# Kernel tuning notes

Measured on AMD Instinct MI355X. Metric: run time of the kernel, lower is better.

## Reference

```python
import jax, jax.numpy as jnp
import numpy as np

N, E, IN, HID, H, C, NL, OUT = 50000, 500000, 384, 128, 8, 16, 3, 16
NEG_SLOPE = 0.2

def setup_inputs() -> dict:
    key = jax.random.key(0)
    ks = jax.random.split(key, 16)
    s = 0.1
    return {
        "x": jax.random.normal(ks[0], (N, IN), jnp.float32),
        "edge_index": jax.random.randint(ks[1], (2, E), 0, N, jnp.int32),
        "proj_w": jax.random.normal(ks[2], (IN, HID), jnp.float32) * s,
        "proj_b": jax.random.normal(ks[3], (HID,), jnp.float32) * s,
        "lin_w": jax.random.normal(ks[4], (NL, HID, HID), jnp.float32) * s,
        "att_src": jax.random.normal(ks[5], (NL, H, C), jnp.float32) * s,
        "att_dst": jax.random.normal(ks[6], (NL, H, C), jnp.float32) * s,
        "gat_b": jax.random.normal(ks[7], (NL, HID), jnp.float32) * s,
        "ln_g": jnp.ones((NL, HID), jnp.float32),
        "ln_b": jnp.zeros((NL, HID), jnp.float32),
        "cls_w1": jax.random.normal(ks[8], (HID, HID // 2), jnp.float32) * s,
        "cls_b1": jax.random.normal(ks[9], (HID // 2,), jnp.float32) * s,
        "cls_w2": jax.random.normal(ks[10], (HID // 2, OUT), jnp.float32) * s,
        "cls_b2": jax.random.normal(ks[11], (OUT,), jnp.float32) * s,
    }

def _layernorm(h, g, b, eps=1e-5):
    mu = jnp.mean(h, axis=-1, keepdims=True)
    var = jnp.var(h, axis=-1, keepdims=True)
    return (h - mu) * jax.lax.rsqrt(var + eps) * g + b

def _gat_layer(h, src, dst, w, a_src, a_dst, bias):
    # h: [N, HID]; per-head transform -> [N, H, C]
    xh = (h @ w).reshape(N, H, C)
    al_s = jnp.einsum('nhc,hc->nh', xh, a_src)   # [N, H]
    al_d = jnp.einsum('nhc,hc->nh', xh, a_dst)
    e = jax.nn.leaky_relu(al_s[src] + al_d[dst], NEG_SLOPE)  # [E+N, H]
    # segment softmax over incoming edges of each dst node
    m = jax.ops.segment_max(e, dst, num_segments=N)
    e = jnp.exp(e - m[dst])
    denom = jax.ops.segment_sum(e, dst, num_segments=N)
    alpha = e / (denom[dst] + 1e-16)
    msg = xh[src] * alpha[:, :, None]            # [E+N, H, C]
    out = jax.ops.segment_sum(msg, dst, num_segments=N)
    return out.reshape(N, H * C) + bias

def reference(x, edge_index, proj_w, proj_b, lin_w, att_src, att_dst, gat_b,
              ln_g, ln_b, cls_w1, cls_b1, cls_w2, cls_b2):
    loops = jnp.arange(N, dtype=edge_index.dtype)  # PyG GATConv adds self-loops
    src = jnp.concatenate([edge_index[0], loops])
    dst = jnp.concatenate([edge_index[1], loops])
    h = jax.nn.relu(x @ proj_w + proj_b)
    for l in range(NL):
        h_res = h
        h = _gat_layer(h, src, dst, lin_w[l], att_src[l], att_dst[l], gat_b[l])
        h = h + h_res
        h = jax.nn.relu(_layernorm(h, ln_g[l], ln_b[l]))
    logits = jax.nn.relu(h @ cls_w1 + cls_b1) @ cls_w2 + cls_b2
    return jax.nn.log_softmax(logits, axis=1)
```

## Files before the change

### kernel.cpp

```cpp
#include <hip/hip_runtime.h>
#include <hip/hip_bf16.h>
#include <math.h>

#define NN 50000
#define EE 500000
#define DIN 384
#define HIDD 128
#define NHEAD 8
#define OUTD 16

typedef __attribute__((ext_vector_type(8))) __bf16 bf16x8;
typedef __attribute__((ext_vector_type(4))) float f32x4;

__device__ __forceinline__ ushort f2bf(float f) {
  union { float f; unsigned u; } v; v.f = f;
  unsigned r = v.u + 0x7fffu + ((v.u >> 16) & 1u);
  return (ushort)(r >> 16);
}
__device__ __forceinline__ float bflo(unsigned w) {
  union { unsigned u; float f; } v; v.u = w << 16; return v.f;
}
__device__ __forceinline__ float bfhi(unsigned w) {
  union { unsigned u; float f; } v; v.u = w & 0xffff0000u; return v.f;
}

__global__ void zero_ints(int* p, int n) {
  int i = blockIdx.x * blockDim.x + threadIdx.x;
  if (i < n) p[i] = 0;
}

__global__ void hist_kernel(const int* __restrict__ dst, int* __restrict__ counts, int e) {
  int i = blockIdx.x * blockDim.x + threadIdx.x;
  if (i < e) atomicAdd(&counts[dst[i]], 1);
}

#define SCAN_BS 256
#define SCAN_NBLK ((NN + SCAN_BS - 1) / SCAN_BS)

__global__ __launch_bounds__(256) void partial_sums(const int* __restrict__ counts,
                                                    int* __restrict__ bsum, int n) {
  __shared__ int red[256];
  int i = blockIdx.x * 256 + threadIdx.x;
  red[threadIdx.x] = (i < n) ? counts[i] : 0;
  __syncthreads();
  #pragma unroll
  for (int off = 128; off; off >>= 1) {
    if (threadIdx.x < off) red[threadIdx.x] += red[threadIdx.x + off];
    __syncthreads();
  }
  if (threadIdx.x == 0) bsum[blockIdx.x] = red[0];
}

__global__ __launch_bounds__(256) void scan_bsums(const int* __restrict__ bsum,
                                                  int* __restrict__ boff, int nb) {
  __shared__ int buf[256];
  int t = threadIdx.x;
  int v = (t < nb) ? bsum[t] : 0;
  buf[t] = v;
  __syncthreads();
  #pragma unroll
  for (int off = 1; off < 256; off <<= 1) {
    int u = (t >= off) ? buf[t - off] : 0;
    __syncthreads();
    buf[t] += u;
    __syncthreads();
  }
  if (t < nb) boff[t] = buf[t] - v;
}

__global__ __launch_bounds__(256) void final_scan(const int* __restrict__ counts,
                                                  const int* __restrict__ boff,
                                                  int* __restrict__ rowptr,
                                                  int* __restrict__ woff, int n) {
  __shared__ int buf[256];
  int i = blockIdx.x * 256 + threadIdx.x;
  int t = threadIdx.x;
  int v = (i < n) ? counts[i] : 0;
  buf[t] = v;
  __syncthreads();
  #pragma unroll
  for (int off = 1; off < 256; off <<= 1) {
    int u = (t >= off) ? buf[t - off] : 0;
    __syncthreads();
    buf[t] += u;
    __syncthreads();
  }
  int excl = boff[blockIdx.x] + buf[t] - v;
  if (i < n) { rowptr[i] = excl; woff[i] = excl; }
  if (i == n - 1) rowptr[n] = excl + v;
}

__global__ void scatter_kernel(const int* __restrict__ src, const int* __restrict__ dst,
                               int* __restrict__ woff, int* __restrict__ col, int e) {
  int i = blockIdx.x * blockDim.x + threadIdx.x;
  if (i < e) {
    int p = atomicAdd(&woff[dst[i]], 1);
    col[p] = src[i];
  }
}

__global__ void prep_weights(const float* __restrict__ proj_w,
                             const float* __restrict__ lin_w,
                             const float* __restrict__ cls_w1,
                             const float* __restrict__ cls_w2,
                             ushort* __restrict__ wt) {
  int i = blockIdx.x * blockDim.x + threadIdx.x;
  if (i < 49152) {
    int k = i >> 7, n = i & 127;
    wt[n * 384 + k] = f2bf(proj_w[i]);
  } else if (i < 98304) {
    int j = i - 49152;
    int l = j >> 14, rem = j & 16383;
    int k = rem >> 7, n = rem & 127;
    wt[49152 + l * 16384 + n * 128 + k] = f2bf(lin_w[j]);
  } else if (i < 106496) {
    int j = i - 98304;
    int n = j >> 7, k = j & 127;
    wt[98304 + n * 128 + k] = f2bf(cls_w1[k * 64 + n]);
  } else if (i < 107520) {
    int j = i - 106496;
    int n = j >> 6, k = j & 63;
    wt[106496 + n * 64 + k] = f2bf(cls_w2[k * 16 + n]);
  }
}

#define LDS_STRIDE 72
template<bool RELU_BIAS, bool OUTBF>
__global__ __launch_bounds__(256) void mfma_gemm_n128(const float* __restrict__ A,
                                                      const ushort* __restrict__ Bt,
                                                      const float* __restrict__ bias,
                                                      void* __restrict__ Cv, int M, int K) {
  __shared__ ushort sA[128 * LDS_STRIDE];
  __shared__ ushort sB[128 * LDS_STRIDE];
  const int tid = threadIdx.x;
  const int wave = tid >> 6, lane = tid & 63;
  const int q = lane >> 4, lm = lane & 15;
  const int wr = wave >> 1, wc = wave & 1;
  const int m0 = blockIdx.x * 128;

  f32x4 acc[4][4];
  #pragma unroll
  for (int i = 0; i < 4; i++)
    #pragma unroll
    for (int j = 0; j < 4; j++) acc[i][j] = {0.f, 0.f, 0.f, 0.f};

  for (int k0 = 0; k0 < K; k0 += 64) {
    __syncthreads();
    #pragma unroll
    for (int p = 0; p < 8; ++p) {
      int idx = p * 256 + tid;
      int r = idx >> 4;
      int c = (idx & 15) << 2;
      float4 v = make_float4(0.f, 0.f, 0.f, 0.f);
      if (m0 + r < M) v = *(const float4*)(A + (size_t)(m0 + r) * K + k0 + c);
      ushort4 u;
      u.x = f2bf(v.x); u.y = f2bf(v.y); u.z = f2bf(v.z); u.w = f2bf(v.w);
      *(ushort4*)&sA[r * LDS_STRIDE + c] = u;
    }
    #pragma unroll
    for (int p = 0; p < 4; ++p) {
      int idx = p * 256 + tid;
      int r = idx >> 3;
      int c = (idx & 7) << 3;
      bf16x8 v = *(const bf16x8*)(Bt + (size_t)r * K + k0 + c);
      *(bf16x8*)&sB[r * LDS_STRIDE + c] = v;
    }
    __syncthreads();
    #pragma unroll
    for (int ks = 0; ks < 2; ++ks) {
      bf16x8 af[4], bfv[4];
      #pragma unroll
      for (int t = 0; t < 4; ++t) {
        af[t]  = *(const bf16x8*)&sA[(wr * 64 + t * 16 + lm) * LDS_STRIDE + ks * 32 + q * 8];
        bfv[t] = *(const bf16x8*)&sB[(wc * 64 + t * 16 + lm) * LDS_STRIDE + ks * 32 + q * 8];
      }
      #pragma unroll
      for (int i = 0; i < 4; ++i)
        #pragma unroll
        for (int j = 0; j < 4; ++j)
          acc[i][j] = __builtin_amdgcn_mfma_f32_16x16x32_bf16(af[i], bfv[j], acc[i][j], 0, 0, 0);
    }
  }
  #pragma unroll
  for (int i = 0; i < 4; ++i) {
    #pragma unroll
    for (int r = 0; r < 4; ++r) {
      int row = m0 + wr * 64 + i * 16 + q * 4 + r;
      if (row < M) {
        #pragma unroll
        for (int j = 0; j < 4; ++j) {
          int colc = wc * 64 + j * 16 + lm;
          float v = acc[i][j][r];
          if (RELU_BIAS) { v += bias[colc]; v = fmaxf(v, 0.f); }
          if (OUTBF) ((ushort*)Cv)[(size_t)row * 128 + colc] = f2bf(v);
          else       ((float*)Cv)[(size_t)row * 128 + colc] = v;
        }
      }
    }
  }
}

__global__ void att_logits_kernel(const ushort* __restrict__ xh,
                                  const float* __restrict__ att_s,
                                  const float* __restrict__ att_d,
                                  float* __restrict__ al_s, float* __restrict__ al_d, int n) {
  int t = blockIdx.x * blockDim.x + threadIdx.x;
  if (t >= n * NHEAD) return;
  int head = t & 7;
  const unsigned* xw = (const unsigned*)(xh + (size_t)t * 16);
  const float* as = att_s + head * 16;
  const float* ad = att_d + head * 16;
  float ss = 0.f, dd = 0.f;
  #pragma unroll
  for (int i = 0; i < 8; ++i) {
    unsigned w = xw[i];
    float x0 = bflo(w), x1 = bfhi(w);
    ss = fmaf(x0, as[i * 2], fmaf(x1, as[i * 2 + 1], ss));
    dd = fmaf(x0, ad[i * 2], fmaf(x1, ad[i * 2 + 1], dd));
  }
  al_s[t] = ss;
  al_d[t] = dd;
}

__global__ __launch_bounds__(256) void gat_aggregate(
    const ushort* __restrict__ xh, const float* __restrict__ al_s,
    const float* __restrict__ al_d, const int* __restrict__ rowptr,
    const int* __restrict__ col, const float* __restrict__ h_res,
    const float* __restrict__ gb, const float* __restrict__ lng,
    const float* __restrict__ lnb, float* __restrict__ h_out, int n) {
  const int lane = threadIdx.x & 63;
  const int node = (blockIdx.x * blockDim.x + threadIdx.x) >> 6;
  if (node >= n) return;
  const int e8 = lane >> 3;
  const int hh = lane & 7;
  const int head = lane >> 3;
  const unsigned* xw_base = (const unsigned*)xh;

  const int start = rowptr[node], end = rowptr[node + 1];
  const int T = end - start + 1;
  const float ald_c = al_d[node * 8 + hh];

  float m = -INFINITY, denom = 0.f, acc0 = 0.f, acc1 = 0.f;

  for (int c = 0; c < T; c += 8) {
    int it = c + e8;
    bool valid = it < T;
    int idx = start + it;
    int s = (valid && idx < end) ? col[idx] : node;
    float e = al_s[s * 8 + hh] + ald_c;
    e = (e > 0.f) ? e : 0.2f * e;
    if (!valid) e = -INFINITY;
    float cm = e;
    cm = fmaxf(cm, __shfl_xor(cm, 8));
    cm = fmaxf(cm, __shfl_xor(cm, 16));
    cm = fmaxf(cm, __shfl_xor(cm, 32));
    float newm = fmaxf(m, __shfl(cm, head));
    float newm_c = __shfl(newm, hh * 8);
    float p_lane = __expf(e - newm_c);
    float scale = __expf(m - newm);
    m = newm;
    unsigned xg[8];
    int sj[8];
    #pragma unroll
    for (int j = 0; j < 8; ++j) sj[j] = __shfl(s, j * 8);
    #pragma unroll
    for (int j = 0; j < 8; ++j) xg[j] = xw_base[(size_t)sj[j] * 64 + lane];
    denom *= scale; acc0 *= scale; acc1 *= scale;
    #pragma unroll
    for (int j = 0; j < 8; ++j) {
      float pj = __shfl(p_lane, j * 8 + head);
      denom += pj;
      acc0 = fmaf(pj, bflo(xg[j]), acc0);
      acc1 = fmaf(pj, bfhi(xg[j]), acc1);
    }
  }

  float inv = 1.f / denom;
  int c0 = lane * 2, c1 = c0 + 1;
  float2 hr = ((const float2*)h_res)[(size_t)node * 64 + lane];
  float v0 = acc0 * inv + gb[c0] + hr.x;
  float v1 = acc1 * inv + gb[c1] + hr.y;
  float sum = v0 + v1;
  #pragma unroll
  for (int off = 32; off; off >>= 1) sum += __shfl_xor(sum, off);
  float mean = sum * (1.f / 128.f);
  float d0 = v0 - mean, d1 = v1 - mean;
  float sq = d0 * d0 + d1 * d1;
  #pragma unroll
  for (int off = 32; off; off >>= 1) sq += __shfl_xor(sq, off);
  float rstd = rsqrtf(sq * (1.f / 128.f) + 1e-5f);
  float o0 = fmaxf(d0 * rstd * lng[c0] + lnb[c0], 0.f);
  float o1 = fmaxf(d1 * rstd * lng[c1] + lnb[c1], 0.f);
  ((float2*)h_out)[(size_t)node * 64 + lane] = make_float2(o0, o1);
}

#define CSTR 136
#define HSTR 72
__global__ __launch_bounds__(256) void classifier_mfma(
    const float* __restrict__ h, const ushort* __restrict__ w1t,
    const float* __restrict__ b1, const ushort* __restrict__ w2t,
    const float* __restrict__ b2, float* __restrict__ out, int n) {
  __shared__ ushort sA[128 * CSTR];
  __shared__ ushort sB[64 * CSTR];
  __shared__ ushort sHid[128 * HSTR];
  const int tid = threadIdx.x;
  const int wave = tid >> 6, lane = tid & 63;
  const int q = lane >> 4, lm = lane & 15;
  const int wr = wave >> 1, wc = wave & 1;
  const int m0 = blockIdx.x * 128;

  #pragma unroll
  for (int p = 0; p < 16; ++p) {
    int idx = p * 256 + tid;
    int r = idx >> 5;
    int c = (idx & 31) << 2;
    float4 v = make_float4(0.f, 0.f, 0.f, 0.f);
    if (m0 + r < n) v = *(const float4*)(h + (size_t)(m0 + r) * 128 + c);
    ushort4 u;
    u.x = f2bf(v.x); u.y = f2bf(v.y); u.z = f2bf(v.z); u.w = f2bf(v.w);
    *(ushort4*)&sA[r * CSTR + c] = u;
  }
  #pragma unroll
  for (int p = 0; p < 4; ++p) {
    int idx = p * 256 + tid;
    int r = idx >> 4;
    int c = (idx & 15) << 3;
    *(bf16x8*)&sB[r * CSTR + c] = *(const bf16x8*)(w1t + r * 128 + c);
  }
  __syncthreads();

  f32x4 acc[4][2];
  #pragma unroll
  for (int i = 0; i < 4; ++i)
    #pragma unroll
    for (int j = 0; j < 2; ++j) acc[i][j] = {0.f, 0.f, 0.f, 0.f};
  #pragma unroll
  for (int ks = 0; ks < 4; ++ks) {
    bf16x8 af[4], bfv[2];
    #pragma unroll
    for (int t = 0; t < 4; ++t)
      af[t] = *(const bf16x8*)&sA[(wr * 64 + t * 16 + lm) * CSTR + ks * 32 + q * 8];
    #pragma unroll
    for (int j = 0; j < 2; ++j)
      bfv[j] = *(const bf16x8*)&sB[(wc * 32 + j * 16 + lm) * CSTR + ks * 32 + q * 8];
    #pragma unroll
    for (int i = 0; i < 4; ++i)
      #pragma unroll
      for (int j = 0; j < 2; ++j)
        acc[i][j] = __builtin_amdgcn_mfma_f32_16x16x32_bf16(af[i], bfv[j], acc[i][j], 0, 0, 0);
  }
  #pragma unroll
  for (int i = 0; i < 4; ++i) {
    #pragma unroll
    for (int j = 0; j < 2; ++j) {
      int colc = wc * 32 + j * 16 + lm;
      float bb = b1[colc];
      #pragma unroll
      for (int r = 0; r < 4; ++r) {
        int row = wr * 64 + i * 16 + q * 4 + r;
        float v = fmaxf(acc[i][j][r] + bb, 0.f);
        sHid[row * HSTR + colc] = f2bf(v);
      }
    }
  }
  __syncthreads();

  f32x4 acc2[2] = {{0.f, 0.f, 0.f, 0.f}, {0.f, 0.f, 0.f, 0.f}};
  #pragma unroll
  for (int ks = 0; ks < 2; ++ks) {
    bf16x8 b2f = *(const bf16x8*)(w2t + lm * 64 + ks * 32 + q * 8);
    #pragma unroll
    for (int t = 0; t < 2; ++t) {
      bf16x8 a2 = *(const bf16x8*)&sHid[(wave * 32 + t * 16 + lm) * HSTR + ks * 32 + q * 8];
      acc2[t] = __builtin_amdgcn_mfma_f32_16x16x32_bf16(a2, b2f, acc2[t], 0, 0, 0);
    }
  }
  float bb2 = b2[lm];
  #pragma unroll
  for (int t = 0; t < 2; ++t) {
    #pragma unroll
    for (int r = 0; r < 4; ++r) {
      int row = m0 + wave * 32 + t * 16 + q * 4 + r;
      float lg = acc2[t][r] + bb2;
      float mx = lg;
      #pragma unroll
      for (int off = 8; off; off >>= 1) mx = fmaxf(mx, __shfl_xor(mx, off, 16));
      float se = __expf(lg - mx);
      #pragma unroll
      for (int off = 8; off; off >>= 1) se += __shfl_xor(se, off, 16);
      if (row < n) out[(size_t)row * 16 + lm] = lg - mx - __logf(se);
    }
  }
}

extern "C" void kernel_launch(void* const* d_in, const int* in_sizes, int n_in,
                              void* d_out, int out_size, void* d_ws, size_t ws_size,
                              hipStream_t stream) {
  const float* x       = (const float*)d_in[0];
  const int*   ei      = (const int*)d_in[1];
  const float* proj_w  = (const float*)d_in[2];
  const float* proj_b  = (const float*)d_in[3];
  const float* lin_w   = (const float*)d_in[4];
  const float* att_src = (const float*)d_in[5];
  const float* att_dst = (const float*)d_in[6];
  const float* gat_b   = (const float*)d_in[7];
  const float* ln_g    = (const float*)d_in[8];
  const float* ln_b    = (const float*)d_in[9];
  const float* cls_w1  = (const float*)d_in[10];
  const float* cls_b1  = (const float*)d_in[11];
  const float* cls_w2  = (const float*)d_in[12];
  const float* cls_b2  = (const float*)d_in[13];
  float* outp = (float*)d_out;

  const int N = NN, E = EE;
  ushort* wt   = (ushort*)d_ws;
  float* h0    = (float*)d_ws + 54272;
  float* h1    = h0 + (size_t)N * 128;
  ushort* xh_u = (ushort*)(h1 + (size_t)N * 128);
  float* als   = (float*)(xh_u + (size_t)N * 128);
  float* ald   = als + (size_t)N * NHEAD;
  int* counts  = (int*)(ald + (size_t)N * NHEAD);
  int* rowptr  = counts + N;
  int* woff    = rowptr + N + 1;
  int* col     = woff + N;
  int* bsum    = col + E;
  int* boff    = bsum + SCAN_NBLK;

  const int* e_src = ei;
  const int* e_dst = ei + E;

  prep_weights<<<(107520 + 255) / 256, 256, 0, stream>>>(proj_w, lin_w, cls_w1, cls_w2, wt);

  zero_ints<<<(N + 255) / 256, 256, 0, stream>>>(counts, N);
  hist_kernel<<<(E + 255) / 256, 256, 0, stream>>>(e_dst, counts, E);
  partial_sums<<<SCAN_NBLK, 256, 0, stream>>>(counts, bsum, N);
  scan_bsums<<<1, 256, 0, stream>>>(bsum, boff, SCAN_NBLK);
  final_scan<<<SCAN_NBLK, 256, 0, stream>>>(counts, boff, rowptr, woff, N);
  scatter_kernel<<<(E + 255) / 256, 256, 0, stream>>>(e_src, e_dst, woff, col, E);

  const int gblocks = (N + 127) / 128;
  mfma_gemm_n128<true, false><<<gblocks, 256, 0, stream>>>(x, wt, proj_b, h0, N, DIN);

  float* hc = h0;
  float* hn = h1;
  for (int l = 0; l < 3; ++l) {
    mfma_gemm_n128<false, true><<<gblocks, 256, 0, stream>>>(
        hc, wt + 49152 + l * 16384, nullptr, xh_u, N, 128);
    att_logits_kernel<<<(N * NHEAD + 255) / 256, 256, 0, stream>>>(
        xh_u, att_src + l * 128, att_dst + l * 128, als, ald, N);
    gat_aggregate<<<(N + 3) / 4, 256, 0, stream>>>(
        xh_u, als, ald, rowptr, col, hc, gat_b + l * 128, ln_g + l * 128,
        ln_b + l * 128, hn, N);
    float* t = hc; hc = hn; hn = t;
  }
  classifier_mfma<<<gblocks, 256, 0, stream>>>(hc, wt + 98304, cls_b1, wt + 106496, cls_b2, outp, N);
}
```

Baseline: 405.8 us.

## Store hidden activations in bf16 and shrink GEMM row tile to 64

Hidden-state buffers h0/h1 are now stored as bf16 instead of fp32, so the GEMMs, the aggregate residual read and output write, and the classifier all move half the bytes. The GEMM kernel is templated on input type and uses a 64-row tile, which doubles the block count for better occupancy across CUs. Out-of-range rows are clamped instead of branched. This adds bf16 rounding on the residual path, which may cost some accuracy.

```diff
diff --git a/kernel.cpp b/kernel.cpp
--- a/kernel.cpp
+++ b/kernel.cpp
@@ -125,75 +125,86 @@
 }
 
 #define LDS_STRIDE 72
-template<bool RELU_BIAS, bool OUTBF>
-__global__ __launch_bounds__(256) void mfma_gemm_n128(const float* __restrict__ A,
-                                                      const ushort* __restrict__ Bt,
-                                                      const float* __restrict__ bias,
-                                                      void* __restrict__ Cv, int M, int K) {
-  __shared__ ushort sA[128 * LDS_STRIDE];
+template<typename AT, bool RELU_BIAS>
+__global__ __launch_bounds__(256) void mfma_gemm64(const AT* __restrict__ A,
+                                                   const ushort* __restrict__ Bt,
+                                                   const float* __restrict__ bias,
+                                                   ushort* __restrict__ C, int M, int K) {
+  __shared__ ushort sA[64 * LDS_STRIDE];
   __shared__ ushort sB[128 * LDS_STRIDE];
   const int tid = threadIdx.x;
   const int wave = tid >> 6, lane = tid & 63;
   const int q = lane >> 4, lm = lane & 15;
   const int wr = wave >> 1, wc = wave & 1;
-  const int m0 = blockIdx.x * 128;
-
-  f32x4 acc[4][4];
-  #pragma unroll
-  for (int i = 0; i < 4; i++)
+  const int m0 = blockIdx.x * 64;
+
+  f32x4 acc[2][4];
+  #pragma unroll
+  for (int i = 0; i < 2; i++)
     #pragma unroll
     for (int j = 0; j < 4; j++) acc[i][j] = {0.f, 0.f, 0.f, 0.f};
 
   for (int k0 = 0; k0 < K; k0 += 64) {
     __syncthreads();
-    #pragma unroll
-    for (int p = 0; p < 8; ++p) {
-      int idx = p * 256 + tid;
-      int r = idx >> 4;
-      int c = (idx & 15) << 2;
-      float4 v = make_float4(0.f, 0.f, 0.f, 0.f);
-      if (m0 + r < M) v = *(const float4*)(A + (size_t)(m0 + r) * K + k0 + c);
-      ushort4 u;
-      u.x = f2bf(v.x); u.y = f2bf(v.y); u.z = f2bf(v.z); u.w = f2bf(v.w);
-      *(ushort4*)&sA[r * LDS_STRIDE + c] = u;
+    if constexpr (sizeof(AT) == 4) {
+      #pragma unroll
+      for (int p = 0; p < 4; ++p) {
+        int idx = p * 256 + tid;
+        int r = idx >> 4;
+        int c = (idx & 15) << 2;
+        int row = min(m0 + r, M - 1);
+        float4 v = *(const float4*)((const float*)A + (size_t)row * K + k0 + c);
+        ushort4 u;
+        u.x = f2bf(v.x); u.y = f2bf(v.y); u.z = f2bf(v.z); u.w = f2bf(v.w);
+        *(ushort4*)&sA[r * LDS_STRIDE + c] = u;
+      }
+    } else {
+      #pragma unroll
+      for (int p = 0; p < 2; ++p) {
+        int idx = p * 256 + tid;
+        int r = idx >> 3;
+        int c = (idx & 7) << 3;
+        int row = min(m0 + r, M - 1);
+        *(bf16x8*)&sA[r * LDS_STRIDE + c] =
+            *(const bf16x8*)((const ushort*)A + (size_t)row * K + k0 + c);
+      }
     }
     #pragma unroll
     for (int p = 0; p < 4; ++p) {
       int idx = p * 256 + tid;
       int r = idx >> 3;
       int c = (idx & 7) << 3;
-      bf16x8 v = *(const bf16x8*)(Bt + (size_t)r * K + k0 + c);
-      *(bf16x8*)&sB[r * LDS_STRIDE + c] = v;
+      *(bf16x8*)&sB[r * LDS_STRIDE + c] = *(const bf16x8*)(Bt + (size_t)r * K + k0 + c);
     }
     __syncthreads();
     #pragma unroll
     for (int ks = 0; ks < 2; ++ks) {
-      bf16x8 af[4], bfv[4];
-      #pragma unroll
-      for (int t = 0; t < 4; ++t) {
-        af[t]  = *(const bf16x8*)&sA[(wr * 64 + t * 16 + lm) * LDS_STRIDE + ks * 32 + q * 8];
+      bf16x8 af[2], bfv[4];
+      #pragma unroll
+      for (int t = 0; t < 2; ++t)
+        af[t] = *(const bf16x8*)&sA[(wr * 32 + t * 16 + lm) * LDS_STRIDE + ks * 32 + q * 8];
+      #pragma unroll
+      for (int t = 0; t < 4; ++t)
         bfv[t] = *(const bf16x8*)&sB[(wc * 64 + t * 16 + lm) * LDS_STRIDE + ks * 32 + q * 8];
-      }
-      #pragma unroll
-      for (int i = 0; i < 4; ++i)
+      #pragma unroll
+      for (int i = 0; i < 2; ++i)
         #pragma unroll
         for (int j = 0; j < 4; ++j)
           acc[i][j] = __builtin_amdgcn_mfma_f32_16x16x32_bf16(af[i], bfv[j], acc[i][j], 0, 0, 0);
     }
   }
   #pragma unroll
-  for (int i = 0; i < 4; ++i) {
+  for (int i = 0; i < 2; ++i) {
     #pragma unroll
     for (int r = 0; r < 4; ++r) {
-      int row = m0 + wr * 64 + i * 16 + q * 4 + r;
+      int row = m0 + wr * 32 + i * 16 + q * 4 + r;
       if (row < M) {
         #pragma unroll
         for (int j = 0; j < 4; ++j) {
           int colc = wc * 64 + j * 16 + lm;
           float v = acc[i][j][r];
           if (RELU_BIAS) { v += bias[colc]; v = fmaxf(v, 0.f); }
-          if (OUTBF) ((ushort*)Cv)[(size_t)row * 128 + colc] = f2bf(v);
-          else       ((float*)Cv)[(size_t)row * 128 + colc] = v;
+          C[(size_t)row * 128 + colc] = f2bf(v);
         }
       }
     }
@@ -225,9 +236,9 @@
 __global__ __launch_bounds__(256) void gat_aggregate(
     const ushort* __restrict__ xh, const float* __restrict__ al_s,
     const float* __restrict__ al_d, const int* __restrict__ rowptr,
-    const int* __restrict__ col, const float* __restrict__ h_res,
+    const int* __restrict__ col, const ushort* __restrict__ h_res,
     const float* __restrict__ gb, const float* __restrict__ lng,
-    const float* __restrict__ lnb, float* __restrict__ h_out, int n) {
+    const float* __restrict__ lnb, ushort* __restrict__ h_out, int n) {
   const int lane = threadIdx.x & 63;
   const int node = (blockIdx.x * blockDim.x + threadIdx.x) >> 6;
   if (node >= n) return;
@@ -277,9 +288,9 @@
 
   float inv = 1.f / denom;
   int c0 = lane * 2, c1 = c0 + 1;
-  float2 hr = ((const float2*)h_res)[(size_t)node * 64 + lane];
-  float v0 = acc0 * inv + gb[c0] + hr.x;
-  float v1 = acc1 * inv + gb[c1] + hr.y;
+  unsigned ur = ((const unsigned*)h_res)[(size_t)node * 64 + lane];
+  float v0 = acc0 * inv + gb[c0] + bflo(ur);
+  float v1 = acc1 * inv + gb[c1] + bfhi(ur);
   float sum = v0 + v1;
   #pragma unroll
   for (int off = 32; off; off >>= 1) sum += __shfl_xor(sum, off);
@@ -291,13 +302,14 @@
   float rstd = rsqrtf(sq * (1.f / 128.f) + 1e-5f);
   float o0 = fmaxf(d0 * rstd * lng[c0] + lnb[c0], 0.f);
   float o1 = fmaxf(d1 * rstd * lng[c1] + lnb[c1], 0.f);
-  ((float2*)h_out)[(size_t)node * 64 + lane] = make_float2(o0, o1);
+  ((unsigned*)h_out)[(size_t)node * 64 + lane] =
+      (unsigned)f2bf(o0) | ((unsigned)f2bf(o1) << 16);
 }
 
 #define CSTR 136
 #define HSTR 72
 __global__ __launch_bounds__(256) void classifier_mfma(
-    const float* __restrict__ h, const ushort* __restrict__ w1t,
+    const ushort* __restrict__ h, const ushort* __restrict__ w1t,
     const float* __restrict__ b1, const ushort* __restrict__ w2t,
     const float* __restrict__ b2, float* __restrict__ out, int n) {
   __shared__ ushort sA[128 * CSTR];
@@ -310,15 +322,12 @@
   const int m0 = blockIdx.x * 128;
 
   #pragma unroll
-  for (int p = 0; p < 16; ++p) {
+  for (int p = 0; p < 8; ++p) {
     int idx = p * 256 + tid;
-    int r = idx >> 5;
-    int c = (idx & 31) << 2;
-    float4 v = make_float4(0.f, 0.f, 0.f, 0.f);
-    if (m0 + r < n) v = *(const float4*)(h + (size_t)(m0 + r) * 128 + c);
-    ushort4 u;
-    u.x = f2bf(v.x); u.y = f2bf(v.y); u.z = f2bf(v.z); u.w = f2bf(v.w);
-    *(ushort4*)&sA[r * CSTR + c] = u;
+    int r = idx >> 4;
+    int c = (idx & 15) << 3;
+    int row = min(m0 + r, n - 1);
+    *(bf16x8*)&sA[r * CSTR + c] = *(const bf16x8*)(h + (size_t)row * 128 + c);
   }
   #pragma unroll
   for (int p = 0; p < 4; ++p) {
@@ -414,9 +423,9 @@
 
   const int N = NN, E = EE;
   ushort* wt   = (ushort*)d_ws;
-  float* h0    = (float*)d_ws + 54272;
-  float* h1    = h0 + (size_t)N * 128;
-  ushort* xh_u = (ushort*)(h1 + (size_t)N * 128);
+  ushort* h0   = wt + 108544;
+  ushort* h1   = h0 + (size_t)N * 128;
+  ushort* xh_u = h1 + (size_t)N * 128;
   float* als   = (float*)(xh_u + (size_t)N * 128);
   float* ald   = als + (size_t)N * NHEAD;
   int* counts  = (int*)(ald + (size_t)N * NHEAD);
@@ -438,20 +447,21 @@
   final_scan<<<SCAN_NBLK, 256, 0, stream>>>(counts, boff, rowptr, woff, N);
   scatter_kernel<<<(E + 255) / 256, 256, 0, stream>>>(e_src, e_dst, woff, col, E);
 
-  const int gblocks = (N + 127) / 128;
-  mfma_gemm_n128<true, false><<<gblocks, 256, 0, stream>>>(x, wt, proj_b, h0, N, DIN);
-
-  float* hc = h0;
-  float* hn = h1;
+  const int gblocks = (N + 63) / 64;
+  mfma_gemm64<float, true><<<gblocks, 256, 0, stream>>>(x, wt, proj_b, h0, N, DIN);
+
+  ushort* hc = h0;
+  ushort* hn = h1;
   for (int l = 0; l < 3; ++l) {
-    mfma_gemm_n128<false, true><<<gblocks, 256, 0, stream>>>(
+    mfma_gemm64<ushort, false><<<gblocks, 256, 0, stream>>>(
         hc, wt + 49152 + l * 16384, nullptr, xh_u, N, 128);
     att_logits_kernel<<<(N * NHEAD + 255) / 256, 256, 0, stream>>>(
         xh_u, att_src + l * 128, att_dst + l * 128, als, ald, N);
     gat_aggregate<<<(N + 3) / 4, 256, 0, stream>>>(
         xh_u, als, ald, rowptr, col, hc, gat_b + l * 128, ln_g + l * 128,
         ln_b + l * 128, hn, N);
-    float* t = hc; hc = hn; hn = t;
-  }
-  classifier_mfma<<<gblocks, 256, 0, stream>>>(hc, wt + 98304, cls_b1, wt + 106496, cls_b2, outp, N);
-}
+    ushort* t = hc; hc = hn; hn = t;
+  }
+  classifier_mfma<<<(N + 127) / 128, 256, 0, stream>>>(
+      hc, wt + 98304, cls_b1, wt + 106496, cls_b2, outp, N);
+}
```

Result: faster. 381.4 us (-6.0%).
